# Kernel optimization log

Hardware: AMD Instinct MI355X
Metric: run time of the kernel (lower is better)

Reference implementation:

```python
import jax, jax.numpy as jnp
import numpy as np

B, L, D, H = 2, 2048, 2048, 16
Dh = D // H
THETA = 500000.0


def _init_rope(dim, seq_len, n_heads):
    # Returns freqs_cis of shape (1, seq_len, 1, head_dim//2, 2) -> [..., 0]=cos, [..., 1]=sin
    hd = dim // n_heads
    inv_freqs = 1.0 / (THETA ** (jnp.arange(0, hd, 2, dtype=jnp.float32) / hd))
    t = jnp.arange(seq_len, dtype=jnp.float32)
    freqs = jnp.outer(t, inv_freqs).astype(jnp.float32)  # (L, hd/2)
    fc = jnp.stack([jnp.cos(freqs)[None, :, None, :],
                    jnp.sin(freqs)[None, :, None, :]], axis=3)  # (1, L, 1, 2, hd/2)
    return fc.transpose(0, 1, 2, 4, 3)  # (1, L, 1, hd/2, 2)


def _apply_rope(q, k, freqs_cis):
    def rotate(x):
        x2 = x.reshape(*x.shape[:-1], -1, 2)  # (B, L, H, Dh/2, 2)
        f = freqs_cis[:, :x.shape[1]]
        cos, sin = f[..., 0], f[..., 1]
        r = jnp.stack([x2[..., 0] * cos - x2[..., 1] * sin,
                       x2[..., 1] * cos + x2[..., 0] * sin], axis=-1)
        return r.reshape(*x.shape)
    return rotate(q), rotate(k)


def setup_inputs() -> dict:
    key = jax.random.key(0)
    kx, kq, kk, kv, ko = jax.random.split(key, 5)
    scale = 1.0 / np.sqrt(D)
    x = jax.random.normal(kx, (B, L, D), dtype=jnp.float32)
    Wq = jax.random.normal(kq, (D, H, Dh), dtype=jnp.float32) * scale
    Wk = jax.random.normal(kk, (D, H, Dh), dtype=jnp.float32) * scale
    Wv = jax.random.normal(kv, (D, H, Dh), dtype=jnp.float32) * scale
    Wo = jax.random.normal(ko, (D, D), dtype=jnp.float32) * scale
    return {"x": x, "Wq": Wq, "Wk": Wk, "Wv": Wv, "Wo": Wo}


def reference(x, Wq, Wk, Wv, Wo):
    freqs_cis = _init_rope(D, L, H)
    q = jnp.einsum('bld,dhk->blhk', x, Wq)  # (B, L, H, Dh)
    k = jnp.einsum('bld,dhk->blhk', x, Wk)
    v = jnp.einsum('bld,dhk->blhk', x, Wv)
    q, k = _apply_rope(q, k, freqs_cis)
    q = q / (Dh ** 0.5)
    att = jnp.einsum('bqhd,bkhd->bhqk', q, k)  # (B, H, L, L)
    Lq = x.shape[1]
    mask = jnp.tril(jnp.ones((1, 1, Lq, Lq), dtype=jnp.bool_))
    neg_inf = jnp.finfo(jnp.float32).min
    att = jnp.where(mask, att, neg_inf)
    att = jax.nn.softmax(att, axis=-1)
    out = jnp.einsum('bhqk,bkhd->bqhd', att, v)  # (B, L, H, Dh)
    out = out.reshape(x.shape)
    return jnp.einsum('bld,de->ble', out, Wo)
```

## Files before the change

### kernel.cpp

```cpp
#include <hip/hip_runtime.h>

typedef unsigned short u16;
typedef unsigned int u32;

#define Bb 2
#define Lc 2048
#define Dc 2048
#define Hc 16
#define DhC 128

typedef __bf16 bf16x8 __attribute__((ext_vector_type(8)));
typedef float f32x4 __attribute__((ext_vector_type(4)));
typedef float f32x16 __attribute__((ext_vector_type(16)));

__device__ __forceinline__ u16 f2b(float f) {
  u32 u = __float_as_uint(f);
  u32 r = (u + 0x7fffu + ((u >> 16) & 1u)) >> 16;
  return (u16)r;
}
__device__ __forceinline__ float b2f(u16 u) {
  return __uint_as_float(((u32)u) << 16);
}

__device__ __forceinline__ u32 cvtpk(float lo, float hi) {
  u32 r;
  asm("v_cvt_pk_bf16_f32 %0, %1, %2" : "=v"(r) : "v"(lo), "v"(hi));
  return r;
}

__device__ __forceinline__ void gll16(const void* g, void* l) {
  __builtin_amdgcn_global_load_lds(
      (const __attribute__((address_space(1))) u32*)g,
      (__attribute__((address_space(3))) u32*)l, 16, 0, 0);
}

__global__ __launch_bounds__(256) void sniff_dtype(const u16* __restrict__ x,
                                                   int* __restrict__ flag) {
  __shared__ int bad;
  if (threadIdx.x == 0) bad = 0;
  __syncthreads();
  int local = 0;
  for (int i = threadIdx.x; i < 65536; i += 256) {
    float v = fabsf(b2f(x[i]));
    if (!(v < 1000.f)) local = 1;
  }
  if (local) atomicOr(&bad, 1);
  __syncthreads();
  if (threadIdx.x == 0) *flag = bad;
}

__global__ __launch_bounds__(256) void conv_x(const void* __restrict__ in,
                                              u16* __restrict__ out,
                                              const int* __restrict__ flag) {
  const int f32 = *flag;
  const int i0 = (blockIdx.x * 256 + threadIdx.x) * 4;
  if (f32) {
    const float* p = (const float*)in;
#pragma unroll
    for (int j = 0; j < 4; j++) out[i0 + j] = f2b(p[i0 + j]);
  } else {
    const u16* p = (const u16*)in;
#pragma unroll
    for (int j = 0; j < 4; j++) out[i0 + j] = p[i0 + j];
  }
}

__device__ __forceinline__ void tconv_body(const void* in, u16* out, int f32) {
  __shared__ __align__(16) u16 tile[64][65];
  const int r0 = blockIdx.y * 64, c0 = blockIdx.x * 64;
  const int tc = threadIdx.x & 63, tr4 = threadIdx.x >> 6;
#pragma unroll
  for (int p = 0; p < 16; p++) {
    int r = tr4 + p * 4;
    size_t idx = (size_t)(r0 + r) * 2048 + c0 + tc;
    tile[r][tc] = f32 ? f2b(((const float*)in)[idx]) : ((const u16*)in)[idx];
  }
  __syncthreads();
#pragma unroll
  for (int p = 0; p < 16; p++) {
    int rr = tr4 + p * 4;
    out[(size_t)(c0 + rr) * 2048 + r0 + tc] = tile[tc][rr];
  }
}

__global__ __launch_bounds__(256) void transpose2d_conv(const void* __restrict__ in,
                                                        u16* __restrict__ out,
                                                        const int* __restrict__ flag) {
  tconv_body(in, out, *flag);
}

__global__ __launch_bounds__(256) void transpose3_conv(const void* __restrict__ W0,
                                                       const void* __restrict__ W1,
                                                       const void* __restrict__ W2,
                                                       u16* __restrict__ out,
                                                       const int* __restrict__ flag) {
  const int z = blockIdx.z;
  const void* in = (z == 0) ? W0 : (z == 1) ? W1 : W2;
  tconv_body(in, out + (size_t)z * 2048 * 2048, *flag);
}

template <typename OutT>
__device__ __forceinline__ void gemmp_core(const u16* __restrict__ A,
                                           const u16* __restrict__ Bt,
                                           OutT* __restrict__ C,
                                           int Ntiles, size_t bufStride) {
  constexpr int K = 2048;
  constexpr int NTK = K / 32;
  __shared__ __align__(16) u16 Als[3][128 * 32];
  __shared__ __align__(16) u16 Bls[3][128 * 32];

  const int tid = threadIdx.x;
  const int lane = tid & 63, w = tid >> 6;
  const int quad = lane >> 4, l15 = lane & 15;
  const int wm = w >> 1, wn = w & 1;

  const int nwg = 32 * Ntiles;
  const int q8 = nwg >> 3;
  const int id = (int)blockIdx.x;
  const int swz = (id & 7) * q8 + (id >> 3);
  const int m0 = (swz & 31) * 128;
  const int n0 = (swz >> 5) * 128;

  const u16* aSrc0 = A + (size_t)(m0 + (2 * w) * 16 + l15) * K + quad * 8;
  const u16* aSrc1 = A + (size_t)(m0 + (2 * w + 1) * 16 + l15) * K + quad * 8;
  const u16* bSrc0 = Bt + (size_t)(n0 + (2 * w) * 16 + l15) * K + quad * 8;
  const u16* bSrc1 = Bt + (size_t)(n0 + (2 * w + 1) * 16 + l15) * K + quad * 8;

  const f32x4 fz = {0.f, 0.f, 0.f, 0.f};
  f32x4 acc[4][4];
#pragma unroll
  for (int i = 0; i < 4; i++)
#pragma unroll
    for (int j = 0; j < 4; j++) acc[i][j] = fz;

  auto stage = [&](int t) {
    const int s = t % 3;
    const int k = t * 32;
    gll16(aSrc0 + k, &Als[s][(2 * w) * 512]);
    gll16(aSrc1 + k, &Als[s][(2 * w + 1) * 512]);
    gll16(bSrc0 + k, &Bls[s][(2 * w) * 512]);
    gll16(bSrc1 + k, &Bls[s][(2 * w + 1) * 512]);
  };

  auto compute = [&](int t) {
    const int s = t % 3;
    bf16x8 afr[4], bfr[4];
#pragma unroll
    for (int mt = 0; mt < 4; mt++)
      afr[mt] = *(const bf16x8*)(&Als[s][(wm * 4 + mt) * 512 + lane * 8]);
#pragma unroll
    for (int nt = 0; nt < 4; nt++)
      bfr[nt] = *(const bf16x8*)(&Bls[s][(wn * 4 + nt) * 512 + lane * 8]);
    asm volatile("s_waitcnt lgkmcnt(0)" ::: "memory");
    __builtin_amdgcn_sched_barrier(0);
    __builtin_amdgcn_s_setprio(1);
#pragma unroll
    for (int mt = 0; mt < 4; mt++)
#pragma unroll
      for (int nt = 0; nt < 4; nt++)
        acc[mt][nt] = __builtin_amdgcn_mfma_f32_16x16x32_bf16(
            afr[mt], bfr[nt], acc[mt][nt], 0, 0, 0);
    __builtin_amdgcn_s_setprio(0);
  };

  stage(0);
  stage(1);
  asm volatile("s_waitcnt vmcnt(4)" ::: "memory");
  __builtin_amdgcn_s_barrier();

  for (int t = 0; t < NTK - 2; ++t) {
    stage(t + 2);
    compute(t);
    asm volatile("s_waitcnt vmcnt(4)" ::: "memory");
    __builtin_amdgcn_s_barrier();
  }
  compute(NTK - 2);
  asm volatile("s_waitcnt vmcnt(0)" ::: "memory");
  __builtin_amdgcn_s_barrier();
  compute(NTK - 1);

#pragma unroll
  for (int mt = 0; mt < 4; mt++)
#pragma unroll
    for (int nt = 0; nt < 4; nt++) {
      const int colg = n0 + wn * 64 + nt * 16 + l15;
      const size_t cbase = (size_t)(colg >> 11) * bufStride + (colg & 2047);
#pragma unroll
      for (int r = 0; r < 4; r++) {
        const int row = m0 + wm * 64 + mt * 16 + quad * 4 + r;
        const float v = acc[mt][nt][r];
        if constexpr (sizeof(OutT) == 2)
          C[cbase + (size_t)row * 2048] = f2b(v);
        else
          C[cbase + (size_t)row * 2048] = v;
      }
    }
}

__global__ __launch_bounds__(256, 4) void gemmp_bf(const u16* __restrict__ A,
                                                   const u16* __restrict__ Bt,
                                                   u16* __restrict__ C,
                                                   int Ntiles, size_t bufStride) {
  gemmp_core<u16>(A, Bt, C, Ntiles, bufStride);
}
__global__ __launch_bounds__(256, 4) void gemmp_f32(const u16* __restrict__ A,
                                                    const u16* __restrict__ Bt,
                                                    float* __restrict__ C,
                                                    int Ntiles, size_t bufStride) {
  gemmp_core<float>(A, Bt, C, Ntiles, bufStride);
}

__global__ __launch_bounds__(256) void transpose_v_k(const u16* __restrict__ V,
                                                     u16* __restrict__ Vt) {
  __shared__ __align__(16) u16 tile[64][65];
  const int z = blockIdx.z;
  const int b = z >> 4, h = z & 15;
  const int l0 = blockIdx.y * 64, d0 = blockIdx.x * 64;
  const int tc = threadIdx.x & 63, tr4 = threadIdx.x >> 6;
#pragma unroll
  for (int p = 0; p < 16; p++) {
    int l = tr4 + p * 4;
    tile[l][tc] = V[(size_t)((b * Lc + l0 + l) * Hc + h) * DhC + d0 + tc];
  }
  __syncthreads();
#pragma unroll
  for (int p = 0; p < 16; p++) {
    int dd = tr4 + p * 4;
    Vt[((size_t)z * DhC + d0 + dd) * Lc + l0 + tc] = tile[tc][dd];
  }
}

__global__ __launch_bounds__(256) void rope_qk(u16* __restrict__ Q, u16* __restrict__ K) {
  const int idx = blockIdx.x * 256 + threadIdx.x;
  const int j = idx & 63;
  const int h = (idx >> 6) & 15;
  const int l = idx >> 10;
  const float inv = exp2f(-0.2958057561f * (float)j);
  const float ang = (float)l * inv;
  float s, c;
  sincosf(ang, &s, &c);
  const float sc = 0.08838834764f;
#pragma unroll
  for (int b = 0; b < Bb; b++) {
    const size_t off = ((size_t)((b * Lc + l) * Hc + h)) * DhC + 2 * j;
    const float q0 = b2f(Q[off]), q1 = b2f(Q[off + 1]);
    const float k0 = b2f(K[off]), k1 = b2f(K[off + 1]);
    Q[off]     = f2b((q0 * c - q1 * s) * sc);
    Q[off + 1] = f2b((q1 * c + q0 * s) * sc);
    K[off]     = f2b(k0 * c - k1 * s);
    K[off + 1] = f2b(k1 * c + k0 * s);
  }
}

#define NEGBIG (-3.0e30f)
__global__ __launch_bounds__(256, 2) void flash_attn(const u16* __restrict__ Q,
                                                     const u16* __restrict__ Kg,
                                                     const u16* __restrict__ Vt,
                                                     u16* __restrict__ O) {
  __shared__ __align__(16) u16 Ks[2][64 * 128];
  __shared__ __align__(16) u16 Vs[2][128 * 64];
  const int tid = threadIdx.x;
  const int lane = tid & 63, w = tid >> 6;
  const int l31 = lane & 31, hib = lane >> 5;
  const int bh = blockIdx.y;
  const int b = bh >> 4, h = bh & 15;
  const int qt = (bh & 16) ? (int)blockIdx.x : (15 - (int)blockIdx.x);
  const int q0 = qt * 128;
  const int qw0 = q0 + w * 32;
  const int nkv = 2 * qt + 2;

  const int krl = lane >> 4, ksl = lane & 15;
  const int vrl = lane >> 3, vsl = lane & 7;

  bf16x8 qf[8];
  {
    const u16* qptr = Q + ((size_t)(b * Lc + qw0 + l31) * Hc + h) * DhC + 8 * hib;
#pragma unroll
    for (int s = 0; s < 8; s++) qf[s] = *(const bf16x8*)(qptr + s * 16);
  }

  {
#pragma unroll
    for (int p = 0; p < 4; p++) {
      const int r = p * 16 + w * 4 + krl;
      const int c = ksl ^ (r & 15);
      gll16(Kg + ((size_t)(b * Lc + r) * Hc + h) * DhC + c * 8,
            &Ks[0][(p * 256 + w * 64) * 8]);
    }
#pragma unroll
    for (int p = 0; p < 4; p++) {
      const int r = p * 32 + w * 8 + vrl;
      const int c = vsl ^ (r & 7);
      gll16(Vt + ((size_t)bh * DhC + r) * Lc + c * 8,
            &Vs[0][(p * 256 + w * 64) * 8]);
    }
  }

  f32x16 o[4];
#pragma unroll
  for (int dt = 0; dt < 4; dt++) o[dt] = (f32x16)0.0f;
  float mrow = NEGBIG, lrow = 0.f;

  __syncthreads();

  for (int kvt = 0; kvt < nkv; kvt++) {
    const int cur = kvt & 1;
    const u16* Ksc = Ks[cur];
    const u16* Vsc = Vs[cur];

    if (kvt + 1 < nkv) {
      const int nv0 = (kvt + 1) * 64;
      const int nxt = cur ^ 1;
#pragma unroll
      for (int p = 0; p < 4; p++) {
        const int r = p * 16 + w * 4 + krl;
        const int c = ksl ^ (r & 15);
        gll16(Kg + ((size_t)(b * Lc + nv0 + r) * Hc + h) * DhC + c * 8,
              &Ks[nxt][(p * 256 + w * 64) * 8]);
      }
#pragma unroll
      for (int p = 0; p < 4; p++) {
        const int r = p * 32 + w * 8 + vrl;
        const int c = vsl ^ (r & 7);
        gll16(Vt + ((size_t)bh * DhC + r) * Lc + nv0 + c * 8,
              &Vs[nxt][(p * 256 + w * 64) * 8]);
      }
    }

    const int kv0 = kvt * 64;
    const bool active = (kv0 <= qw0 + 31);
    if (active) {
      f32x16 s0 = (f32x16)0.0f, s1 = (f32x16)0.0f;
      __builtin_amdgcn_s_setprio(1);
#pragma unroll
      for (int s = 0; s < 8; s++) {
        const int ch = ((2 * s + hib) ^ (l31 & 15)) * 8;
        bf16x8 k0 = *(const bf16x8*)(&Ksc[l31 * 128 + ch]);
        bf16x8 k1 = *(const bf16x8*)(&Ksc[(32 + l31) * 128 + ch]);
        s0 = __builtin_amdgcn_mfma_f32_32x32x16_bf16(k0, qf[s], s0, 0, 0, 0);
        s1 = __builtin_amdgcn_mfma_f32_32x32x16_bf16(k1, qf[s], s1, 0, 0, 0);
      }
      __builtin_amdgcn_s_setprio(0);

      if (kv0 + 63 > qw0) {
        const int qg = qw0 + l31;
#pragma unroll
        for (int r = 0; r < 16; r++) {
          const int cr = (r & 3) + 8 * (r >> 2) + 4 * hib;
          if (kv0 + cr > qg) s0[r] = NEGBIG;
          if (kv0 + 32 + cr > qg) s1[r] = NEGBIG;
        }
      }

      float mx;
      {
        float a[8];
#pragma unroll
        for (int i = 0; i < 8; i++)
          a[i] = fmaxf(fmaxf(s0[i], s0[i + 8]), fmaxf(s1[i], s1[i + 8]));
        float b0 = fmaxf(a[0], a[4]), b1 = fmaxf(a[1], a[5]);
        float b2 = fmaxf(a[2], a[6]), b3 = fmaxf(a[3], a[7]);
        mx = fmaxf(fmaxf(b0, b1), fmaxf(b2, b3));
      }
      mx = fmaxf(mx, __shfl_xor(mx, 32, 64));

      if (!__all(mx - mrow <= 8.f)) {
        const float mnew = fmaxf(mrow, mx);
        const float al = __expf(mrow - mnew);
#pragma unroll
        for (int dt = 0; dt < 4; dt++)
#pragma unroll
          for (int e = 0; e < 16; e++) o[dt][e] *= al;
        lrow *= al;
        mrow = mnew;
      }

#pragma unroll
      for (int i = 0; i < 16; i++) {
        s0[i] = __expf(s0[i] - mrow);
        s1[i] = __expf(s1[i] - mrow);
      }
      float sm;
      {
        float a[8];
#pragma unroll
        for (int i = 0; i < 8; i++)
          a[i] = (s0[i] + s0[i + 8]) + (s1[i] + s1[i + 8]);
        sm = ((a[0] + a[4]) + (a[1] + a[5])) + ((a[2] + a[6]) + (a[3] + a[7]));
      }
      sm += __shfl_xor(sm, 32, 64);
      lrow += sm;

      bf16x8 paf[4];
#pragma unroll
      for (int t = 0; t < 2; t++) {
#pragma unroll
        for (int h8 = 0; h8 < 2; h8++) {
          const int rB = 8 * h8;
          u32 lo0, lo1, hi0, hi1;
          if (t == 0) {
            lo0 = cvtpk(s0[rB + 0], s0[rB + 1]);
            lo1 = cvtpk(s0[rB + 2], s0[rB + 3]);
            hi0 = cvtpk(s0[rB + 4], s0[rB + 5]);
            hi1 = cvtpk(s0[rB + 6], s0[rB + 7]);
          } else {
            lo0 = cvtpk(s1[rB + 0], s1[rB + 1]);
            lo1 = cvtpk(s1[rB + 2], s1[rB + 3]);
            hi0 = cvtpk(s1[rB + 4], s1[rB + 5]);
            hi1 = cvtpk(s1[rB + 6], s1[rB + 7]);
          }
          const u32 g0 = hib ? lo0 : hi0;
          const u32 g1 = hib ? lo1 : hi1;
          const u32 r0 = (u32)__shfl_xor((int)g0, 32, 64);
          const u32 r1 = (u32)__shfl_xor((int)g1, 32, 64);
          union { u32 u[4]; bf16x8 v; } pu;
          pu.u[0] = hib ? r0 : lo0;
          pu.u[1] = hib ? r1 : lo1;
          pu.u[2] = hib ? hi0 : r0;
          pu.u[3] = hib ? hi1 : r1;
          paf[2 * t + h8] = pu.v;
        }
      }

      __builtin_amdgcn_s_setprio(1);
#pragma unroll
      for (int B = 0; B < 4; B++) {
#pragma unroll
        for (int dt = 0; dt < 4; dt++) {
          const bf16x8 vf = *(const bf16x8*)(
              &Vsc[(32 * dt + l31) * 64 + (((2 * B + hib) ^ (l31 & 7))) * 8]);
          o[dt] = __builtin_amdgcn_mfma_f32_32x32x16_bf16(paf[B], vf, o[dt], 0, 0, 0);
        }
      }
      __builtin_amdgcn_s_setprio(0);
    }

    __syncthreads();
  }

#pragma unroll
  for (int r = 0; r < 16; r++) {
    const int cr = (r & 3) + 8 * (r >> 2) + 4 * hib;
    const float linv = 1.0f / __shfl(lrow, cr, 64);
    const size_t rowoff = ((size_t)(b * Lc + qw0 + cr) * Hc + h) * DhC + l31;
#pragma unroll
    for (int dt = 0; dt < 4; dt++)
      O[rowoff + 32 * dt] = f2b(o[dt][r] * linv);
  }
}

extern "C" void kernel_launch(void* const* d_in, const int* in_sizes, int n_in,
                              void* d_out, int out_size, void* d_ws, size_t ws_size,
                              hipStream_t stream) {
  const void* x  = d_in[0];
  const void* Wq = d_in[1];
  const void* Wk = d_in[2];
  const void* Wv = d_in[3];
  const void* Wo = d_in[4];
  float* out = (float*)d_out;

  char* w = (char*)d_ws;
  const size_t WSZ = (size_t)2048 * 2048;
  const size_t XSZ = (size_t)Bb * Lc * Dc;
  int* flag = (int*)w;
  u16* WT  = (u16*)(w + 256);
  u16* xc  = WT + WSZ;
  u16* Qb  = xc + XSZ;
  u16* Kb  = Qb + XSZ;
  u16* Vb  = Kb + XSZ;
  u16* Vtb = xc;
  u16* Ob  = Vb;
  u16* WTall = (u16*)d_out;

  sniff_dtype<<<1, 256, 0, stream>>>((const u16*)x, flag);
  conv_x<<<(int)(XSZ / 1024), 256, 0, stream>>>(x, xc, flag);

  transpose3_conv<<<dim3(32, 32, 3), 256, 0, stream>>>(Wq, Wk, Wv, WTall, flag);

  gemmp_bf<<<dim3(1536), 256, 0, stream>>>(xc, WTall, Qb, 48, XSZ);

  rope_qk<<<(Lc * Hc * 64) / 256, 256, 0, stream>>>(Qb, Kb);

  dim3 vgrid(2, 32, 32);
  transpose_v_k<<<vgrid, 256, 0, stream>>>(Vb, Vtb);

  dim3 fgrid(16, 32);
  flash_attn<<<fgrid, 256, 0, stream>>>(Qb, Kb, Vtb, Ob);

  dim3 tgrid(32, 32);
  transpose2d_conv<<<tgrid, 256, 0, stream>>>(Wo, WT, flag);
  gemmp_f32<<<dim3(512), 256, 0, stream>>>(Ob, WT, out, 16, 0);
}
```

Before: 572.1 us.

## Enlarge GEMM tiles to 256x256 with 512-thread blocks and unrolled triple buffer

Replaces the 128x128, 256-thread projection GEMM with a 512-thread kernel using 256x256 tiles for the fused QKV projection and 256x128 tiles for the output projection. The three-stage LDS ring is unrolled by three so buffer indices are compile-time constants, and the vmcnt waits are adjusted to match the per-stage load count. The larger tiles raise arithmetic intensity and cut global and LDS traffic per MFMA. In exchange there are fewer blocks (384 and 256 on a large-CU GPU), one block per CU, and higher register and LDS pressure, which reduces latency hiding.

Result: faster. 531.1 us (-7.2%).

```diff
diff --git a/kernel.cpp b/kernel.cpp
--- a/kernel.cpp
+++ b/kernel.cpp
@@ -99,95 +99,106 @@
   tconv_body(in, out + (size_t)z * 2048 * 2048, *flag);
 }
 
-template <typename OutT>
-__device__ __forceinline__ void gemmp_core(const u16* __restrict__ A,
+template <typename OutT, int BN>
+__device__ __forceinline__ void g256f_core(const u16* __restrict__ A,
                                            const u16* __restrict__ Bt,
                                            OutT* __restrict__ C,
-                                           int Ntiles, size_t bufStride) {
+                                           int nwg, size_t bufStride) {
   constexpr int K = 2048;
-  constexpr int NTK = K / 32;
-  __shared__ __align__(16) u16 Als[3][128 * 32];
-  __shared__ __align__(16) u16 Bls[3][128 * 32];
+  constexpr int WNW = (BN == 256) ? 4 : 2;
+  constexpr int MT = (BN == 256) ? 8 : 4;
+  constexpr int NT = 4;
+  __shared__ __align__(16) u16 Asl[3][256 * 32];
+  __shared__ __align__(16) u16 Bsl[3][BN * 32];
 
   const int tid = threadIdx.x;
   const int lane = tid & 63, w = tid >> 6;
   const int quad = lane >> 4, l15 = lane & 15;
-  const int wm = w >> 1, wn = w & 1;
-
-  const int nwg = 32 * Ntiles;
+  const int wm = w / WNW, wn = w % WNW;
+
   const int q8 = nwg >> 3;
   const int id = (int)blockIdx.x;
   const int swz = (id & 7) * q8 + (id >> 3);
-  const int m0 = (swz & 31) * 128;
-  const int n0 = (swz >> 5) * 128;
-
-  const u16* aSrc0 = A + (size_t)(m0 + (2 * w) * 16 + l15) * K + quad * 8;
-  const u16* aSrc1 = A + (size_t)(m0 + (2 * w + 1) * 16 + l15) * K + quad * 8;
-  const u16* bSrc0 = Bt + (size_t)(n0 + (2 * w) * 16 + l15) * K + quad * 8;
-  const u16* bSrc1 = Bt + (size_t)(n0 + (2 * w + 1) * 16 + l15) * K + quad * 8;
+  const int m0 = (swz & 15) * 256;
+  const int n0 = (swz >> 4) * BN;
+
+  const u16* aS = A + (size_t)(m0 + w * 16 + l15) * K + quad * 8;
+  const u16* bS = Bt + (size_t)(n0 + w * 16 + l15) * K + quad * 8;
 
   const f32x4 fz = {0.f, 0.f, 0.f, 0.f};
-  f32x4 acc[4][4];
-#pragma unroll
-  for (int i = 0; i < 4; i++)
-#pragma unroll
-    for (int j = 0; j < 4; j++) acc[i][j] = fz;
-
-  auto stage = [&](int t) {
-    const int s = t % 3;
-    const int k = t * 32;
-    gll16(aSrc0 + k, &Als[s][(2 * w) * 512]);
-    gll16(aSrc1 + k, &Als[s][(2 * w + 1) * 512]);
-    gll16(bSrc0 + k, &Bls[s][(2 * w) * 512]);
-    gll16(bSrc1 + k, &Bls[s][(2 * w + 1) * 512]);
+  f32x4 acc[MT][NT];
+#pragma unroll
+  for (int i = 0; i < MT; i++)
+#pragma unroll
+    for (int j = 0; j < NT; j++) acc[i][j] = fz;
+
+  auto stagef = [&](int kidx, int sl) {
+    const int kk = kidx * 32;
+    gll16(aS + kk, &Asl[sl][w * 512]);
+    gll16(aS + (size_t)128 * K + kk, &Asl[sl][(8 + w) * 512]);
+    gll16(bS + kk, &Bsl[sl][w * 512]);
+    if constexpr (BN == 256)
+      gll16(bS + (size_t)128 * K + kk, &Bsl[sl][(8 + w) * 512]);
   };
 
-  auto compute = [&](int t) {
-    const int s = t % 3;
-    bf16x8 afr[4], bfr[4];
-#pragma unroll
-    for (int mt = 0; mt < 4; mt++)
-      afr[mt] = *(const bf16x8*)(&Als[s][(wm * 4 + mt) * 512 + lane * 8]);
-#pragma unroll
-    for (int nt = 0; nt < 4; nt++)
-      bfr[nt] = *(const bf16x8*)(&Bls[s][(wn * 4 + nt) * 512 + lane * 8]);
+  auto computef = [&](int sl) {
+    bf16x8 afr[MT], bfr[NT];
+#pragma unroll
+    for (int mt = 0; mt < MT; mt++)
+      afr[mt] = *(const bf16x8*)(&Asl[sl][(wm * MT + mt) * 512 + lane * 8]);
+#pragma unroll
+    for (int nt = 0; nt < NT; nt++)
+      bfr[nt] = *(const bf16x8*)(&Bsl[sl][(wn * NT + nt) * 512 + lane * 8]);
     asm volatile("s_waitcnt lgkmcnt(0)" ::: "memory");
     __builtin_amdgcn_sched_barrier(0);
     __builtin_amdgcn_s_setprio(1);
 #pragma unroll
-    for (int mt = 0; mt < 4; mt++)
-#pragma unroll
-      for (int nt = 0; nt < 4; nt++)
+    for (int mt = 0; mt < MT; mt++)
+#pragma unroll
+      for (int nt = 0; nt < NT; nt++)
         acc[mt][nt] = __builtin_amdgcn_mfma_f32_16x16x32_bf16(
             afr[mt], bfr[nt], acc[mt][nt], 0, 0, 0);
     __builtin_amdgcn_s_setprio(0);
   };
 
-  stage(0);
-  stage(1);
-  asm volatile("s_waitcnt vmcnt(4)" ::: "memory");
+#define GVW()                                                                \
+  do {                                                                       \
+    if constexpr (BN == 256)                                                 \
+      asm volatile("s_waitcnt vmcnt(4)" ::: "memory");                       \
+    else                                                                     \
+      asm volatile("s_waitcnt vmcnt(3)" ::: "memory");                       \
+  } while (0)
+
+  stagef(0, 0);
+  stagef(1, 1);
+  GVW();
   __builtin_amdgcn_s_barrier();
 
-  for (int t = 0; t < NTK - 2; ++t) {
-    stage(t + 2);
-    compute(t);
-    asm volatile("s_waitcnt vmcnt(4)" ::: "memory");
-    __builtin_amdgcn_s_barrier();
-  }
-  compute(NTK - 2);
+  int t = 0;
+#pragma unroll 1
+  for (int c = 0; c < 20; ++c) {
+    stagef(t + 2, 2); computef(0); GVW(); __builtin_amdgcn_s_barrier();
+    stagef(t + 3, 0); computef(1); GVW(); __builtin_amdgcn_s_barrier();
+    stagef(t + 4, 1); computef(2); GVW(); __builtin_amdgcn_s_barrier();
+    t += 3;
+  }
+  stagef(62, 2); computef(0); GVW(); __builtin_amdgcn_s_barrier();
+  stagef(63, 0); computef(1); GVW(); __builtin_amdgcn_s_barrier();
+  computef(2);
   asm volatile("s_waitcnt vmcnt(0)" ::: "memory");
   __builtin_amdgcn_s_barrier();
-  compute(NTK - 1);
-
-#pragma unroll
-  for (int mt = 0; mt < 4; mt++)
-#pragma unroll
-    for (int nt = 0; nt < 4; nt++) {
+  computef(0);
+#undef GVW
+
+#pragma unroll
+  for (int mt = 0; mt < MT; mt++)
+#pragma unroll
+    for (int nt = 0; nt < NT; nt++) {
       const int colg = n0 + wn * 64 + nt * 16 + l15;
       const size_t cbase = (size_t)(colg >> 11) * bufStride + (colg & 2047);
 #pragma unroll
       for (int r = 0; r < 4; r++) {
-        const int row = m0 + wm * 64 + mt * 16 + quad * 4 + r;
+        const int row = m0 + wm * (MT * 16) + mt * 16 + quad * 4 + r;
         const float v = acc[mt][nt][r];
         if constexpr (sizeof(OutT) == 2)
           C[cbase + (size_t)row * 2048] = f2b(v);
@@ -197,17 +208,17 @@
     }
 }
 
-__global__ __launch_bounds__(256, 4) void gemmp_bf(const u16* __restrict__ A,
+__global__ __launch_bounds__(512, 1) void g256f_bf(const u16* __restrict__ A,
                                                    const u16* __restrict__ Bt,
                                                    u16* __restrict__ C,
-                                                   int Ntiles, size_t bufStride) {
-  gemmp_core<u16>(A, Bt, C, Ntiles, bufStride);
-}
-__global__ __launch_bounds__(256, 4) void gemmp_f32(const u16* __restrict__ A,
+                                                   int nwg, size_t bufStride) {
+  g256f_core<u16, 256>(A, Bt, C, nwg, bufStride);
+}
+__global__ __launch_bounds__(512, 1) void g256f_f32(const u16* __restrict__ A,
                                                     const u16* __restrict__ Bt,
                                                     float* __restrict__ C,
-                                                    int Ntiles, size_t bufStride) {
-  gemmp_core<float>(A, Bt, C, Ntiles, bufStride);
+                                                    int nwg, size_t bufStride) {
+  g256f_core<float, 128>(A, Bt, C, nwg, bufStride);
 }
 
 __global__ __launch_bounds__(256) void transpose_v_k(const u16* __restrict__ V,
@@ -477,7 +488,7 @@
 
   transpose3_conv<<<dim3(32, 32, 3), 256, 0, stream>>>(Wq, Wk, Wv, WTall, flag);
 
-  gemmp_bf<<<dim3(1536), 256, 0, stream>>>(xc, WTall, Qb, 48, XSZ);
+  g256f_bf<<<dim3(384), 512, 0, stream>>>(xc, WTall, Qb, 384, XSZ);
 
   rope_qk<<<(Lc * Hc * 64) / 256, 256, 0, stream>>>(Qb, Kb);
 
@@ -489,5 +500,5 @@
 
   dim3 tgrid(32, 32);
   transpose2d_conv<<<tgrid, 256, 0, stream>>>(Wo, WT, flag);
-  gemmp_f32<<<dim3(512), 256, 0, stream>>>(Ob, WT, out, 16, 0);
-}
+  g256f_f32<<<dim3(256), 512, 0, stream>>>(Ob, WT, out, 256, 0);
+}
```
